# Optimization experiments

Hardware: AMD Instinct MI355X
Metric: run time of the kernel (lower is better)

Reference implementation:

```python
import jax, jax.numpy as jnp
import numpy as np

N_NODES = 100000
N_EDGES = 1600000
IN_DIM = 128
LATENT = [128, 128, 16]  # last entry = num classes (logits dim)


def setup_inputs() -> dict:
    key = jax.random.key(0)
    ks = jax.random.split(key, 16)
    inp = {
        "x": jax.random.normal(ks[0], (N_NODES, IN_DIM), dtype=jnp.float32),
        "edge_index": jax.random.randint(ks[1], (2, N_EDGES), 0, N_NODES, dtype=jnp.int64),
        "edge_weight": jax.random.uniform(ks[2], (N_EDGES,), dtype=jnp.float32),
    }
    dims = [IN_DIM] + LATENT
    for i in range(len(LATENT)):
        fan_in = dims[i]
        scale = 1.0 / np.sqrt(fan_in)
        inp[f"W{i}"] = jax.random.uniform(ks[3 + 2 * i], (dims[i], dims[i + 1]), minval=-scale, maxval=scale, dtype=jnp.float32)
        inp[f"b{i}"] = jax.random.uniform(ks[4 + 2 * i], (dims[i + 1],), minval=-scale, maxval=scale, dtype=jnp.float32)
        inp[f"eps{i}"] = jnp.zeros((), dtype=jnp.float32)  # GINConv train_eps init = 0
    return inp


def _gin_layer(x, W, b, eps, src, dst, edge_weight):
    # message: x_j (optionally scaled by edge weight), summed into target nodes
    msg = x[src]
    if edge_weight is not None:
        msg = msg * edge_weight[:, None]
    agg = jax.ops.segment_sum(msg, dst, num_segments=N_NODES)
    h = (1.0 + eps) * x + agg
    return jax.nn.relu(h @ W + b)  # MLP = Linear + ReLU


def _l2_normalize(x, eps=1e-12):
    norm = jnp.linalg.norm(x, axis=-1, keepdims=True)
    return x / jnp.maximum(norm, eps)


def reference(x, edge_index, edge_weight, W0, b0, eps0, W1, b1, eps1, W2, b2, eps2):
    src, dst = edge_index[0], edge_index[1]
    params = [(W0, b0, eps0), (W1, b1, eps1), (W2, b2, eps2)]
    h = x
    # all but last layer: GINConv(with edge_weight) -> l2 normalize -> ReLU
    for (W, b, e) in params[:-1]:
        h = _gin_layer(h, W, b, e, src, dst, edge_weight)
        h = _l2_normalize(h)  # emb_normlize=True
        h = jax.nn.relu(h)
    # last layer: GINConv WITHOUT edge_weight (forward passes only x, edge_index)
    W, b, e = params[-1]
    logits = _gin_layer(h, W, b, e, src, dst, None)
    probs = jax.nn.softmax(logits, axis=-1)
    return (logits, probs)
```

## Files before the change

### kernel.cpp

```cpp
#include <hip/hip_runtime.h>
#include <hip/hip_bf16.h>

#define N_NODES 100000
#define N_EDGES 1600000
#define DIM 128
#define ODIM 16
#define NB 391
#define PCHUNK 3200
#define PBLK 500
#define FCAP 6144

typedef unsigned int uint32;
typedef float f32x4 __attribute__((ext_vector_type(4)));
typedef short bf16x8 __attribute__((ext_vector_type(8)));

static __device__ __forceinline__ float bflo(uint32 p) { return __uint_as_float(p << 16); }
static __device__ __forceinline__ float bfhi(uint32 p) { return __uint_as_float(p & 0xFFFF0000u); }
static __device__ __forceinline__ unsigned short f2bf(float f) {
  __hip_bfloat16 h = __float2bfloat16(f);
  return *reinterpret_cast<unsigned short*>(&h);
}
static __device__ __forceinline__ uint32 pk2bf(float a, float b) {
  return (uint32)f2bf(a) | ((uint32)f2bf(b) << 16);
}

__global__ __launch_bounds__(256) void bucket_hist_kernel(
    const int* __restrict__ dst, int* __restrict__ bcnt) {
  __shared__ int h[NB];
  int tid = threadIdx.x;
  for (int i = tid; i < NB; i += 256) h[i] = 0;
  __syncthreads();
  int e0 = blockIdx.x * PCHUNK;
  for (int i = tid; i < PCHUNK; i += 256) atomicAdd(&h[dst[e0 + i] >> 8], 1);
  __syncthreads();
  for (int i = tid; i < NB; i += 256)
    if (h[i]) atomicAdd(&bcnt[i], h[i]);
}

__global__ __launch_bounds__(512) void bucket_scan_kernel(
    const int* __restrict__ bcnt, int* __restrict__ bbase,
    int* __restrict__ bcur) {
  __shared__ int sc[512];
  int t = threadIdx.x;
  int v = (t < NB) ? bcnt[t] : 0;
  sc[t] = v;
  __syncthreads();
  for (int off = 1; off < 512; off <<= 1) {
    int a = (t >= off) ? sc[t - off] : 0;
    __syncthreads();
    sc[t] += a;
    __syncthreads();
  }
  if (t < NB) {
    int base = sc[t] - v;
    bbase[t] = base;
    bcur[t] = base;
  }
}

__global__ __launch_bounds__(256) void coarse_partition_kernel(
    const int* __restrict__ src, const int* __restrict__ dst,
    const float* __restrict__ ew, int* __restrict__ bcur,
    int2* __restrict__ epack) {
  __shared__ int hist[NB];
  __shared__ int base_a[NB];
  __shared__ int lcur_a[NB];
  __shared__ int gbase_a[NB];
  __shared__ int2 stg[PCHUNK];
  __shared__ int gpos[PCHUNK];

  int tid = threadIdx.x;
  int e0 = blockIdx.x * PCHUNK;

  for (int i = tid; i < NB; i += 256) hist[i] = 0;
  __syncthreads();
  for (int i = tid; i < PCHUNK; i += 256) atomicAdd(&hist[dst[e0 + i] >> 8], 1);
  __syncthreads();

  if (tid < 64) {
    int run = 0;
#pragma unroll
    for (int c = 0; c < 7; c++) {
      int idx = c * 64 + tid;
      int v = (idx < NB) ? hist[idx] : 0;
      int incl = v;
#pragma unroll
      for (int off = 1; off < 64; off <<= 1) {
        int tv = __shfl_up(incl, off, 64);
        if (tid >= off) incl += tv;
      }
      if (idx < NB) base_a[idx] = run + incl - v;
      run += __shfl(incl, 63, 64);
    }
  }
  __syncthreads();
  for (int i = tid; i < NB; i += 256) {
    int c = hist[i];
    gbase_a[i] = (c > 0) ? atomicAdd(&bcur[i], c) : 0;
    lcur_a[i] = base_a[i];
  }
  __syncthreads();

  for (int i = tid; i < PCHUNK; i += 256) {
    int e = e0 + i;
    int s = src[e], d = dst[e];
    float w = ew[e];
    int b = d >> 8;
    int pos = atomicAdd(&lcur_a[b], 1);
    stg[pos] = make_int2(s | ((d & 255) << 20), __float_as_int(w));
    gpos[pos] = gbase_a[b] + (pos - base_a[b]);
  }
  __syncthreads();
  for (int i = tid; i < PCHUNK; i += 256) epack[gpos[i]] = stg[i];
}

__global__ __launch_bounds__(256) void fine_sort_kernel(
    const int* __restrict__ bbase, int2* __restrict__ epack,
    int* __restrict__ row_ptr) {
  __shared__ int2 ebuf[FCAP];
  __shared__ int hist[256];
  __shared__ int sc[256];
  __shared__ int cur[256];
  int tid = threadIdx.x;
  int b = blockIdx.x;
  int node0 = b << 8;
  int lo = bbase[b];
  int hi = (b == NB - 1) ? N_EDGES : bbase[b + 1];
  int n = hi - lo;
  if (n > FCAP) n = FCAP;
  hist[tid] = 0;
  __syncthreads();
  for (int i = tid; i < n; i += 256) {
    int2 e = epack[lo + i];
    ebuf[i] = e;
    atomicAdd(&hist[(e.x >> 20) & 255], 1);
  }
  __syncthreads();
  sc[tid] = hist[tid];
  __syncthreads();
  for (int off = 1; off < 256; off <<= 1) {
    int a = (tid >= off) ? sc[tid - off] : 0;
    __syncthreads();
    sc[tid] += a;
    __syncthreads();
  }
  int rp = lo + sc[tid] - hist[tid];
  if (node0 + tid < N_NODES) row_ptr[node0 + tid] = rp;
  cur[tid] = rp;
  if (b == 0 && tid == 0) row_ptr[N_NODES] = N_EDGES;
  __syncthreads();
  for (int i = tid; i < n; i += 256) {
    int2 e = ebuf[i];
    int pos = atomicAdd(&cur[(e.x >> 20) & 255], 1);
    epack[pos] = make_int2(e.x & 0xFFFFF, e.y);
  }
}

__global__ __launch_bounds__(256) void cast_x_kernel(
    const float2* __restrict__ x2, uint32* __restrict__ Xu) {
  int i = blockIdx.x * 256 + threadIdx.x;
  if (i < N_NODES * (DIM / 2)) {
    float2 v = x2[i];
    Xu[i] = pk2bf(v.x, v.y);
  }
}

__global__ __launch_bounds__(256) void packW128_kernel(
    const float* __restrict__ W, unsigned short* __restrict__ out) {
  int idx = blockIdx.x * 256 + threadIdx.x;
  int j = idx & 7, lane = (idx >> 3) & 63, nt = (idx >> 9) & 7, kc = idx >> 12;
  int k = kc * 32 + (lane >> 4) * 8 + j;
  int n = nt * 16 + (lane & 15);
  out[idx] = f2bf(W[k * DIM + n]);
}

__global__ __launch_bounds__(256) void packW16_kernel(
    const float* __restrict__ W, unsigned short* __restrict__ out) {
  int idx = blockIdx.x * 256 + threadIdx.x;
  if (idx >= 2048) return;
  int j = idx & 7, lane = (idx >> 3) & 63, kc = idx >> 9;
  int k = kc * 32 + (lane >> 4) * 8 + j;
  int n = lane & 15;
  out[idx] = f2bf(W[k * ODIM + n]);
}

__global__ __launch_bounds__(256) void gather_bf16(
    const uint32* __restrict__ hu, const int* __restrict__ row_ptr,
    const int2* __restrict__ ep, uint32* __restrict__ aggu) {
  int lane = threadIdx.x & 63;
  int node = blockIdx.x * 4 + (threadIdx.x >> 6);
  if (node >= N_NODES) return;
  int grp = lane >> 4, l4 = lane & 15;
  int a = row_ptr[node], bnd = row_ptr[node + 1];
  float acc[8];
#pragma unroll
  for (int k = 0; k < 8; k++) acc[k] = 0.f;

  auto pass4 = [&](int jj) {
    int2 e = ep[jj + grp];
    uint4 p = *(const uint4*)(hu + (size_t)e.x * 64 + l4 * 4);
    float wv = __int_as_float(e.y);
    acc[0] = fmaf(wv, bflo(p.x), acc[0]); acc[1] = fmaf(wv, bfhi(p.x), acc[1]);
    acc[2] = fmaf(wv, bflo(p.y), acc[2]); acc[3] = fmaf(wv, bfhi(p.y), acc[3]);
    acc[4] = fmaf(wv, bflo(p.z), acc[4]); acc[5] = fmaf(wv, bfhi(p.z), acc[5]);
    acc[6] = fmaf(wv, bflo(p.w), acc[6]); acc[7] = fmaf(wv, bfhi(p.w), acc[7]);
  };

  int j = a;
  for (; j + 8 <= bnd; j += 8) { pass4(j); pass4(j + 4); }
  if (j + 4 <= bnd) { pass4(j); j += 4; }
  if (j < bnd) {
    int idx = j + grp;
    int vld = idx < bnd;
    int2 e = ep[vld ? idx : bnd - 1];
    uint4 p = *(const uint4*)(hu + (size_t)e.x * 64 + l4 * 4);
    float wv = vld ? __int_as_float(e.y) : 0.f;
    acc[0] = fmaf(wv, bflo(p.x), acc[0]); acc[1] = fmaf(wv, bfhi(p.x), acc[1]);
    acc[2] = fmaf(wv, bflo(p.y), acc[2]); acc[3] = fmaf(wv, bfhi(p.y), acc[3]);
    acc[4] = fmaf(wv, bflo(p.z), acc[4]); acc[5] = fmaf(wv, bfhi(p.z), acc[5]);
    acc[6] = fmaf(wv, bflo(p.w), acc[6]); acc[7] = fmaf(wv, bfhi(p.w), acc[7]);
  }
#pragma unroll
  for (int k = 0; k < 8; k++) {
    acc[k] += __shfl_xor(acc[k], 16, 64);
    acc[k] += __shfl_xor(acc[k], 32, 64);
  }
  if (lane < 16) {
    uint4 st = {pk2bf(acc[0], acc[1]), pk2bf(acc[2], acc[3]),
                pk2bf(acc[4], acc[5]), pk2bf(acc[6], acc[7])};
    *(uint4*)(aggu + (size_t)node * 64 + l4 * 4) = st;
  }
}

template <int FUSE_PROJ>
__global__ __launch_bounds__(256) void gin_mlp_mfma(
    const uint32* Xu, const uint32* __restrict__ Au,
    const unsigned char* __restrict__ pW, const float* __restrict__ b,
    const float* __restrict__ eps_p, uint32* outH,
    const unsigned char* __restrict__ pW2, float* __restrict__ y) {
  __shared__ __align__(16) unsigned char smem[17408 + 32768];
  unsigned char* As = smem;
  unsigned char* Bs = smem + 17408;

  int tid = threadIdx.x;
  int node0 = blockIdx.x * 64;
  float epf = 1.0f + *eps_p;

  for (int i = tid; i < 64 * 64; i += 256) {
    int n = i >> 6, fp = i & 63;
    int node = node0 + n;
    int cn = node < N_NODES ? node : N_NODES - 1;
    size_t idx = (size_t)cn * 64 + fp;
    uint32 xv = Xu[idx], av = Au[idx];
    float u0 = fmaf(epf, bflo(xv), bflo(av));
    float u1 = fmaf(epf, bfhi(xv), bfhi(av));
    *(uint32*)(As + n * 272 + fp * 4) = pk2bf(u0, u1);
  }
  {
    const uint4* Wp = (const uint4*)pW;
    uint4* Bl = (uint4*)Bs;
    for (int i = tid; i < 2048; i += 256) Bl[i] = Wp[i];
  }
  __syncthreads();

  int w = tid >> 6, l = tid & 63;
  int m = l & 15, q = l >> 4;

  f32x4 acc[8];
#pragma unroll
  for (int nt = 0; nt < 8; nt++) acc[nt] = (f32x4){0.f, 0.f, 0.f, 0.f};

  const unsigned char* Abase = As + (w * 16 + m) * 272 + q * 16;
  const unsigned char* Bbase = Bs + l * 16;
#pragma unroll
  for (int kc = 0; kc < 4; kc++) {
    bf16x8 af = *(const bf16x8*)(Abase + kc * 64);
#pragma unroll
    for (int nt = 0; nt < 8; nt++) {
      bf16x8 bfr = *(const bf16x8*)(Bbase + (kc * 8 + nt) * 1024);
      acc[nt] = __builtin_amdgcn_mfma_f32_16x16x32_bf16(af, bfr, acc[nt], 0, 0, 0);
    }
  }

  float ss[4] = {0.f, 0.f, 0.f, 0.f};
#pragma unroll
  for (int nt = 0; nt < 8; nt++) {
    float bj = b[nt * 16 + m];
#pragma unroll
    for (int r = 0; r < 4; r++) {
      float v = fmaxf(acc[nt][r] + bj, 0.0f);
      acc[nt][r] = v;
      ss[r] += v * v;
    }
  }
#pragma unroll
  for (int r = 0; r < 4; r++) {
    float s = ss[r];
    s += __shfl_xor(s, 1, 64);
    s += __shfl_xor(s, 2, 64);
    s += __shfl_xor(s, 4, 64);
    s += __shfl_xor(s, 8, 64);
    ss[r] = 1.0f / fmaxf(sqrtf(s), 1e-12f);
  }
  __syncthreads();
#pragma unroll
  for (int nt = 0; nt < 8; nt++) {
#pragma unroll
    for (int r = 0; r < 4; r++) {
      unsigned short hv = f2bf(acc[nt][r] * ss[r]);
      *(unsigned short*)(As + (w * 16 + q * 4 + r) * 272 + (nt * 16 + m) * 2) = hv;
    }
  }
  __syncthreads();
  int rem = N_NODES - node0; if (rem > 64) rem = 64;
  for (int i = tid; i < 1024; i += 256) {
    int row = i >> 4, seg = i & 15;
    if (row < rem) {
      uint4 vv = *(const uint4*)(As + row * 272 + seg * 16);
      *(uint4*)((unsigned char*)outH + (size_t)(node0 + row) * 256 + seg * 16) = vv;
    }
  }
  if (FUSE_PROJ) {
    f32x4 accy = (f32x4){0.f, 0.f, 0.f, 0.f};
#pragma unroll
    for (int kc = 0; kc < 4; kc++) {
      bf16x8 af = *(const bf16x8*)(Abase + kc * 64);
      bf16x8 bfr = *(const bf16x8*)(pW2 + (size_t)(kc * 64 + l) * 16);
      accy = __builtin_amdgcn_mfma_f32_16x16x32_bf16(af, bfr, accy, 0, 0, 0);
    }
#pragma unroll
    for (int r = 0; r < 4; r++) {
      int orow = node0 + w * 16 + q * 4 + r;
      if (orow < N_NODES) y[(size_t)orow * ODIM + m] = accy[r];
    }
  }
}

__global__ __launch_bounds__(256) void gather16_final_kernel(
    const float* __restrict__ y, const int* __restrict__ row_ptr,
    const int2* __restrict__ ep, const float* __restrict__ b,
    const float* __restrict__ eps_p, float* __restrict__ out_logits,
    float* __restrict__ out_probs) {
  int lane = threadIdx.x & 63;
  int node = blockIdx.x * 4 + (threadIdx.x >> 6);
  if (node >= N_NODES) return;
  int f = lane & 15, eq = lane >> 4;
  int a = row_ptr[node], bnd = row_ptr[node + 1];
  float acc = 0.0f;
  int j = a + eq;
  for (; j + 8 <= bnd; j += 8) {
    int s0 = ep[j].x, s1 = ep[j + 4].x;
    acc += y[(size_t)s0 * ODIM + f] + y[(size_t)s1 * ODIM + f];
  }
  for (; j < bnd; j += 4) acc += y[(size_t)ep[j].x * ODIM + f];
  acc += __shfl_xor(acc, 16, 64);
  acc += __shfl_xor(acc, 32, 64);
  if (eq == 0) {
    float epf = 1.0f + *eps_p;
    size_t idx = (size_t)node * ODIM + f;
    float logit = fmaxf(fmaf(epf, y[idx], acc) + b[f], 0.0f);
    float mx = logit;
#pragma unroll
    for (int mm = 8; mm >= 1; mm >>= 1) mx = fmaxf(mx, __shfl_xor(mx, mm, 16));
    float e = __expf(logit - mx);
    float ssum = e;
#pragma unroll
    for (int mm = 8; mm >= 1; mm >>= 1) ssum += __shfl_xor(ssum, mm, 16);
    out_logits[idx] = logit;
    out_probs[idx] = e / ssum;
  }
}

extern "C" void kernel_launch(void* const* d_in, const int* in_sizes, int n_in,
                              void* d_out, int out_size, void* d_ws, size_t ws_size,
                              hipStream_t stream) {
  const float* x = (const float*)d_in[0];
  const int* ei = (const int*)d_in[1];
  const float* ew = (const float*)d_in[2];
  const float* W0 = (const float*)d_in[3];
  const float* b0 = (const float*)d_in[4];
  const float* e0 = (const float*)d_in[5];
  const float* W1 = (const float*)d_in[6];
  const float* b1 = (const float*)d_in[7];
  const float* e1 = (const float*)d_in[8];
  const float* W2 = (const float*)d_in[9];
  const float* b2 = (const float*)d_in[10];
  const float* e2 = (const float*)d_in[11];
  float* out = (float*)d_out;

  const int* srcp = ei;
  const int* dstp = ei + N_EDGES;

  char* ws = (char*)d_ws;
  size_t off = 0;
  uint32* Agg = (uint32*)(ws + off);  off += (size_t)N_NODES * DIM * 2;
  uint32* Xb  = (uint32*)(ws + off);  off += (size_t)N_NODES * DIM * 2;
  uint32* H   = (uint32*)(ws + off);  off += (size_t)N_NODES * DIM * 2;
  int2* epack = (int2*)(ws + off);    off += (size_t)N_EDGES * 8;
  float* y    = (float*)(ws + off);   off += (size_t)N_NODES * ODIM * 4;
  int* row_ptr = (int*)(ws + off);    off += (size_t)(N_NODES + 16) * 4;
  int* bcnt   = (int*)(ws + off);     off += 2048;
  int* bbase  = (int*)(ws + off);     off += 2048;
  int* bcur   = (int*)(ws + off);     off += 2048;
  unsigned short* pW0 = (unsigned short*)(ws + off); off += 32768;
  unsigned short* pW1 = (unsigned short*)(ws + off); off += 32768;
  unsigned short* pW2 = (unsigned short*)(ws + off); off += 4096;

  cast_x_kernel<<<(N_NODES * (DIM / 2) + 255) / 256, 256, 0, stream>>>(
      (const float2*)x, Xb);
  packW128_kernel<<<64, 256, 0, stream>>>(W0, pW0);
  packW128_kernel<<<64, 256, 0, stream>>>(W1, pW1);
  packW16_kernel<<<8, 256, 0, stream>>>(W2, pW2);

  hipMemsetAsync(bcnt, 0, NB * sizeof(int), stream);
  bucket_hist_kernel<<<PBLK, 256, 0, stream>>>(dstp, bcnt);
  bucket_scan_kernel<<<1, 512, 0, stream>>>(bcnt, bbase, bcur);
  coarse_partition_kernel<<<PBLK, 256, 0, stream>>>(srcp, dstp, ew, bcur, epack);
  fine_sort_kernel<<<NB, 256, 0, stream>>>(bbase, epack, row_ptr);

  int ggrid = (N_NODES + 3) / 4;
  int mgrid = (N_NODES + 63) / 64;

  gather_bf16<<<ggrid, 256, 0, stream>>>(Xb, row_ptr, epack, Agg);
  gin_mlp_mfma<0><<<mgrid, 256, 0, stream>>>(Xb, Agg, (const unsigned char*)pW0,
                                             b0, e0, H, nullptr, nullptr);
  gather_bf16<<<ggrid, 256, 0, stream>>>(H, row_ptr, epack, Agg);
  gin_mlp_mfma<1><<<mgrid, 256, 0, stream>>>(H, Agg, (const unsigned char*)pW1,
                                             b1, e1, H,
                                             (const unsigned char*)pW2, y);
  gather16_final_kernel<<<ggrid, 256, 0, stream>>>(y, row_ptr, epack, b2, e2,
                                                   out, out + (size_t)N_NODES * ODIM);
}
```

Measured before the change: 402.6 us.

## Fuse neighbor gather with MFMA MLP into one kernel per GIN layer

Each GIN layer's edge gather is merged into the MLP kernel. Every wavefront aggregates its 16 nodes one at a time, adds the (1+eps)-scaled self feature, and writes the result straight into the shared-memory A tile. This removes the Agg intermediate's global write and read and one launch per layer, and ping-pongs between two H buffers. Weight fragments are now read from global memory instead of being staged in LDS. The cost is much less parallelism in the gather: one 256-thread block now covers 64 nodes serially per wave instead of 4 nodes, which may hide gather latency worse and unbalance work.

```diff
diff --git a/kernel.cpp b/kernel.cpp
--- a/kernel.cpp
+++ b/kernel.cpp
@@ -184,101 +184,91 @@
   out[idx] = f2bf(W[k * ODIM + n]);
 }
 
-__global__ __launch_bounds__(256) void gather_bf16(
-    const uint32* __restrict__ hu, const int* __restrict__ row_ptr,
-    const int2* __restrict__ ep, uint32* __restrict__ aggu) {
-  int lane = threadIdx.x & 63;
-  int node = blockIdx.x * 4 + (threadIdx.x >> 6);
-  if (node >= N_NODES) return;
-  int grp = lane >> 4, l4 = lane & 15;
-  int a = row_ptr[node], bnd = row_ptr[node + 1];
-  float acc[8];
-#pragma unroll
-  for (int k = 0; k < 8; k++) acc[k] = 0.f;
-
-  auto pass4 = [&](int jj) {
-    int2 e = ep[jj + grp];
-    uint4 p = *(const uint4*)(hu + (size_t)e.x * 64 + l4 * 4);
-    float wv = __int_as_float(e.y);
-    acc[0] = fmaf(wv, bflo(p.x), acc[0]); acc[1] = fmaf(wv, bfhi(p.x), acc[1]);
-    acc[2] = fmaf(wv, bflo(p.y), acc[2]); acc[3] = fmaf(wv, bfhi(p.y), acc[3]);
-    acc[4] = fmaf(wv, bflo(p.z), acc[4]); acc[5] = fmaf(wv, bfhi(p.z), acc[5]);
-    acc[6] = fmaf(wv, bflo(p.w), acc[6]); acc[7] = fmaf(wv, bfhi(p.w), acc[7]);
-  };
-
-  int j = a;
-  for (; j + 8 <= bnd; j += 8) { pass4(j); pass4(j + 4); }
-  if (j + 4 <= bnd) { pass4(j); j += 4; }
-  if (j < bnd) {
-    int idx = j + grp;
-    int vld = idx < bnd;
-    int2 e = ep[vld ? idx : bnd - 1];
-    uint4 p = *(const uint4*)(hu + (size_t)e.x * 64 + l4 * 4);
-    float wv = vld ? __int_as_float(e.y) : 0.f;
-    acc[0] = fmaf(wv, bflo(p.x), acc[0]); acc[1] = fmaf(wv, bfhi(p.x), acc[1]);
-    acc[2] = fmaf(wv, bflo(p.y), acc[2]); acc[3] = fmaf(wv, bfhi(p.y), acc[3]);
-    acc[4] = fmaf(wv, bflo(p.z), acc[4]); acc[5] = fmaf(wv, bfhi(p.z), acc[5]);
-    acc[6] = fmaf(wv, bflo(p.w), acc[6]); acc[7] = fmaf(wv, bfhi(p.w), acc[7]);
-  }
-#pragma unroll
-  for (int k = 0; k < 8; k++) {
-    acc[k] += __shfl_xor(acc[k], 16, 64);
-    acc[k] += __shfl_xor(acc[k], 32, 64);
-  }
-  if (lane < 16) {
-    uint4 st = {pk2bf(acc[0], acc[1]), pk2bf(acc[2], acc[3]),
-                pk2bf(acc[4], acc[5]), pk2bf(acc[6], acc[7])};
-    *(uint4*)(aggu + (size_t)node * 64 + l4 * 4) = st;
-  }
-}
-
 template <int FUSE_PROJ>
-__global__ __launch_bounds__(256) void gin_mlp_mfma(
-    const uint32* Xu, const uint32* __restrict__ Au,
-    const unsigned char* __restrict__ pW, const float* __restrict__ b,
-    const float* __restrict__ eps_p, uint32* outH,
+__global__ __launch_bounds__(256) void gin_fused(
+    const uint32* __restrict__ Hin, const int* __restrict__ row_ptr,
+    const int2* __restrict__ ep, const unsigned char* __restrict__ pW,
+    const float* __restrict__ b, const float* __restrict__ eps_p,
+    uint32* __restrict__ Hout,
     const unsigned char* __restrict__ pW2, float* __restrict__ y) {
-  __shared__ __align__(16) unsigned char smem[17408 + 32768];
-  unsigned char* As = smem;
-  unsigned char* Bs = smem + 17408;
-
+  __shared__ __align__(16) unsigned char As[64 * 272];
   int tid = threadIdx.x;
   int node0 = blockIdx.x * 64;
+  int w = tid >> 6, l = tid & 63;
+  int grp = l >> 4, l4 = l & 15;
   float epf = 1.0f + *eps_p;
-
-  for (int i = tid; i < 64 * 64; i += 256) {
-    int n = i >> 6, fp = i & 63;
-    int node = node0 + n;
+  int nbase = node0 + w * 16;
+
+  int rpl;
+  {
+    int qi = nbase + (l < 17 ? l : 16);
+    qi = qi < N_NODES ? qi : N_NODES;
+    rpl = row_ptr[qi];
+  }
+
+#pragma unroll 1
+  for (int n = 0; n < 16; n++) {
+    int a = __shfl(rpl, n, 64);
+    int bnd = __shfl(rpl, n + 1, 64);
+    float acc[8];
+#pragma unroll
+    for (int k = 0; k < 8; k++) acc[k] = 0.f;
+
+    auto pass4 = [&](int jj) {
+      int2 e = ep[jj + grp];
+      uint4 p = *(const uint4*)(Hin + (size_t)e.x * 64 + l4 * 4);
+      float wv = __int_as_float(e.y);
+      acc[0] = fmaf(wv, bflo(p.x), acc[0]); acc[1] = fmaf(wv, bfhi(p.x), acc[1]);
+      acc[2] = fmaf(wv, bflo(p.y), acc[2]); acc[3] = fmaf(wv, bfhi(p.y), acc[3]);
+      acc[4] = fmaf(wv, bflo(p.z), acc[4]); acc[5] = fmaf(wv, bfhi(p.z), acc[5]);
+      acc[6] = fmaf(wv, bflo(p.w), acc[6]); acc[7] = fmaf(wv, bfhi(p.w), acc[7]);
+    };
+
+    int j = a;
+#pragma unroll 1
+    for (; j + 8 <= bnd; j += 8) { pass4(j); pass4(j + 4); }
+    if (j + 4 <= bnd) { pass4(j); j += 4; }
+    if (j < bnd) {
+      int idx = j + grp;
+      int vld = idx < bnd;
+      int2 e = ep[vld ? idx : bnd - 1];
+      uint4 p = *(const uint4*)(Hin + (size_t)e.x * 64 + l4 * 4);
+      float wv = vld ? __int_as_float(e.y) : 0.f;
+      acc[0] = fmaf(wv, bflo(p.x), acc[0]); acc[1] = fmaf(wv, bfhi(p.x), acc[1]);
+      acc[2] = fmaf(wv, bflo(p.y), acc[2]); acc[3] = fmaf(wv, bfhi(p.y), acc[3]);
+      acc[4] = fmaf(wv, bflo(p.z), acc[4]); acc[5] = fmaf(wv, bfhi(p.z), acc[5]);
+      acc[6] = fmaf(wv, bflo(p.w), acc[6]); acc[7] = fmaf(wv, bfhi(p.w), acc[7]);
+    }
+#pragma unroll
+    for (int k = 0; k < 8; k++) {
+      acc[k] += __shfl_xor(acc[k], 16, 64);
+      acc[k] += __shfl_xor(acc[k], 32, 64);
+    }
+    int node = nbase + n;
     int cn = node < N_NODES ? node : N_NODES - 1;
-    size_t idx = (size_t)cn * 64 + fp;
-    uint32 xv = Xu[idx], av = Au[idx];
-    float u0 = fmaf(epf, bflo(xv), bflo(av));
-    float u1 = fmaf(epf, bfhi(xv), bfhi(av));
-    *(uint32*)(As + n * 272 + fp * 4) = pk2bf(u0, u1);
-  }
-  {
-    const uint4* Wp = (const uint4*)pW;
-    uint4* Bl = (uint4*)Bs;
-    for (int i = tid; i < 2048; i += 256) Bl[i] = Wp[i];
-  }
-  __syncthreads();
-
-  int w = tid >> 6, l = tid & 63;
+    uint4 own = *(const uint4*)(Hin + (size_t)cn * 64 + l4 * 4);
+    uint32 o0 = pk2bf(fmaf(epf, bflo(own.x), acc[0]), fmaf(epf, bfhi(own.x), acc[1]));
+    uint32 o1 = pk2bf(fmaf(epf, bflo(own.y), acc[2]), fmaf(epf, bfhi(own.y), acc[3]));
+    uint32 o2 = pk2bf(fmaf(epf, bflo(own.z), acc[4]), fmaf(epf, bfhi(own.z), acc[5]));
+    uint32 o3 = pk2bf(fmaf(epf, bflo(own.w), acc[6]), fmaf(epf, bfhi(own.w), acc[7]));
+    if (l < 16) {
+      uint4 st = {o0, o1, o2, o3};
+      *(uint4*)(As + (w * 16 + n) * 272 + l4 * 16) = st;
+    }
+  }
+
   int m = l & 15, q = l >> 4;
-
-  f32x4 acc[8];
-#pragma unroll
-  for (int nt = 0; nt < 8; nt++) acc[nt] = (f32x4){0.f, 0.f, 0.f, 0.f};
-
+  f32x4 acc2[8];
+#pragma unroll
+  for (int nt = 0; nt < 8; nt++) acc2[nt] = (f32x4){0.f, 0.f, 0.f, 0.f};
   const unsigned char* Abase = As + (w * 16 + m) * 272 + q * 16;
-  const unsigned char* Bbase = Bs + l * 16;
 #pragma unroll
   for (int kc = 0; kc < 4; kc++) {
     bf16x8 af = *(const bf16x8*)(Abase + kc * 64);
 #pragma unroll
     for (int nt = 0; nt < 8; nt++) {
-      bf16x8 bfr = *(const bf16x8*)(Bbase + (kc * 8 + nt) * 1024);
-      acc[nt] = __builtin_amdgcn_mfma_f32_16x16x32_bf16(af, bfr, acc[nt], 0, 0, 0);
+      bf16x8 bfr = *(const bf16x8*)(pW + (size_t)((kc * 8 + nt) * 64 + l) * 16);
+      acc2[nt] = __builtin_amdgcn_mfma_f32_16x16x32_bf16(af, bfr, acc2[nt], 0, 0, 0);
     }
   }
 
@@ -288,8 +278,8 @@
     float bj = b[nt * 16 + m];
 #pragma unroll
     for (int r = 0; r < 4; r++) {
-      float v = fmaxf(acc[nt][r] + bj, 0.0f);
-      acc[nt][r] = v;
+      float v = fmaxf(acc2[nt][r] + bj, 0.0f);
+      acc2[nt][r] = v;
       ss[r] += v * v;
     }
   }
@@ -302,36 +292,37 @@
     s += __shfl_xor(s, 8, 64);
     ss[r] = 1.0f / fmaxf(sqrtf(s), 1e-12f);
   }
-  __syncthreads();
 #pragma unroll
   for (int nt = 0; nt < 8; nt++) {
 #pragma unroll
     for (int r = 0; r < 4; r++) {
-      unsigned short hv = f2bf(acc[nt][r] * ss[r]);
+      unsigned short hv = f2bf(acc2[nt][r] * ss[r]);
       *(unsigned short*)(As + (w * 16 + q * 4 + r) * 272 + (nt * 16 + m) * 2) = hv;
     }
   }
+
+  if (FUSE_PROJ) {
+    f32x4 accy = (f32x4){0.f, 0.f, 0.f, 0.f};
+#pragma unroll
+    for (int kc = 0; kc < 4; kc++) {
+      bf16x8 af = *(const bf16x8*)(Abase + kc * 64);
+      bf16x8 bfr = *(const bf16x8*)(pW2 + (size_t)(kc * 64 + l) * 16);
+      accy = __builtin_amdgcn_mfma_f32_16x16x32_bf16(af, bfr, accy, 0, 0, 0);
+    }
+#pragma unroll
+    for (int r = 0; r < 4; r++) {
+      int orow = node0 + w * 16 + q * 4 + r;
+      if (orow < N_NODES) y[(size_t)orow * ODIM + m] = accy[r];
+    }
+  }
+
   __syncthreads();
   int rem = N_NODES - node0; if (rem > 64) rem = 64;
   for (int i = tid; i < 1024; i += 256) {
     int row = i >> 4, seg = i & 15;
     if (row < rem) {
       uint4 vv = *(const uint4*)(As + row * 272 + seg * 16);
-      *(uint4*)((unsigned char*)outH + (size_t)(node0 + row) * 256 + seg * 16) = vv;
-    }
-  }
-  if (FUSE_PROJ) {
-    f32x4 accy = (f32x4){0.f, 0.f, 0.f, 0.f};
-#pragma unroll
-    for (int kc = 0; kc < 4; kc++) {
-      bf16x8 af = *(const bf16x8*)(Abase + kc * 64);
-      bf16x8 bfr = *(const bf16x8*)(pW2 + (size_t)(kc * 64 + l) * 16);
-      accy = __builtin_amdgcn_mfma_f32_16x16x32_bf16(af, bfr, accy, 0, 0, 0);
-    }
-#pragma unroll
-    for (int r = 0; r < 4; r++) {
-      int orow = node0 + w * 16 + q * 4 + r;
-      if (orow < N_NODES) y[(size_t)orow * ODIM + m] = accy[r];
+      *(uint4*)((unsigned char*)Hout + (size_t)(node0 + row) * 256 + seg * 16) = vv;
     }
   }
 }
@@ -393,9 +384,9 @@
 
   char* ws = (char*)d_ws;
   size_t off = 0;
-  uint32* Agg = (uint32*)(ws + off);  off += (size_t)N_NODES * DIM * 2;
   uint32* Xb  = (uint32*)(ws + off);  off += (size_t)N_NODES * DIM * 2;
-  uint32* H   = (uint32*)(ws + off);  off += (size_t)N_NODES * DIM * 2;
+  uint32* H0  = (uint32*)(ws + off);  off += (size_t)N_NODES * DIM * 2;
+  uint32* H1  = (uint32*)(ws + off);  off += (size_t)N_NODES * DIM * 2;
   int2* epack = (int2*)(ws + off);    off += (size_t)N_EDGES * 8;
   float* y    = (float*)(ws + off);   off += (size_t)N_NODES * ODIM * 4;
   int* row_ptr = (int*)(ws + off);    off += (size_t)(N_NODES + 16) * 4;
@@ -418,16 +409,15 @@
   coarse_partition_kernel<<<PBLK, 256, 0, stream>>>(srcp, dstp, ew, bcur, epack);
   fine_sort_kernel<<<NB, 256, 0, stream>>>(bbase, epack, row_ptr);
 
+  int mgrid = (N_NODES + 63) / 64;
   int ggrid = (N_NODES + 3) / 4;
-  int mgrid = (N_NODES + 63) / 64;
-
-  gather_bf16<<<ggrid, 256, 0, stream>>>(Xb, row_ptr, epack, Agg);
-  gin_mlp_mfma<0><<<mgrid, 256, 0, stream>>>(Xb, Agg, (const unsigned char*)pW0,
-                                             b0, e0, H, nullptr, nullptr);
-  gather_bf16<<<ggrid, 256, 0, stream>>>(H, row_ptr, epack, Agg);
-  gin_mlp_mfma<1><<<mgrid, 256, 0, stream>>>(H, Agg, (const unsigned char*)pW1,
-                                             b1, e1, H,
-                                             (const unsigned char*)pW2, y);
+
+  gin_fused<0><<<mgrid, 256, 0, stream>>>(Xb, row_ptr, epack,
+                                          (const unsigned char*)pW0, b0, e0,
+                                          H0, nullptr, nullptr);
+  gin_fused<1><<<mgrid, 256, 0, stream>>>(H0, row_ptr, epack,
+                                          (const unsigned char*)pW1, b1, e1,
+                                          H1, (const unsigned char*)pW2, y);
   gather16_final_kernel<<<ggrid, 256, 0, stream>>>(y, row_ptr, epack, b2, e2,
                                                    out, out + (size_t)N_NODES * ODIM);
 }
```

Result: slower. 431.8 us (+7.3%).
